# Optimization experiments

Hardware: AMD Instinct MI355X
Metric: run time of the kernel (lower is better)

## Reference

```python
import jax, jax.numpy as jnp
import numpy as np

B, T, C = 2, 2048, 2048
NH, NKVH = 16, 4
HS = C // NH  # 128
NEG_INF = -1e30


def _rope_freqs(T, hs, base=10000.0):
    inv = 1.0 / (base ** (np.arange(0, hs, 2, dtype=np.float32) / hs))  # [hs/2]
    ang = np.arange(T, dtype=np.float32)[:, None] * inv[None, :]        # [T, hs/2]
    return jnp.asarray(np.cos(ang)), jnp.asarray(np.sin(ang))


def setup_inputs() -> dict:
    key = jax.random.key(0)
    ks = jax.random.split(key, 4)
    x = jax.random.normal(ks[0], (B, T, C), dtype=jnp.float32)
    W_attn = jax.random.normal(ks[1], (C, C + 2 * NKVH * HS), dtype=jnp.float32) * 0.02
    b_attn = jnp.zeros((C + 2 * NKVH * HS,), dtype=jnp.float32)
    W_proj = jax.random.normal(ks[2], (C, C), dtype=jnp.float32) * 0.02
    b_proj = jnp.zeros((C,), dtype=jnp.float32)
    freqs_cos, freqs_sin = _rope_freqs(T, HS)
    return {"x": x, "freqs_cos": freqs_cos, "freqs_sin": freqs_sin,
            "W_attn": W_attn, "b_attn": b_attn, "W_proj": W_proj, "b_proj": b_proj}


def _apply_rope(x, cos, sin):
    # x: [B, T, H, hs]; cos/sin: [T, hs/2] -> broadcast [1, T, 1, hs/2]
    b, t, h, hs = x.shape
    x_ = x.reshape(b, t, h, hs // 2, 2)
    re, im = x_[..., 0], x_[..., 1]
    c = cos[None, :, None, :]
    s = sin[None, :, None, :]
    out_re = re * c - im * s
    out_im = re * s + im * c
    return jnp.stack([out_re, out_im], axis=-1).reshape(b, t, h, hs)


def reference(x, freqs_cos, freqs_sin, W_attn, b_attn, W_proj, b_proj):
    b, t, c = x.shape
    qkv = x @ W_attn + b_attn                                   # [B,T,C+2*nkvh*hs]
    q, k, v = jnp.split(qkv, [c, c + NKVH * HS], axis=2)
    q = q.reshape(b, t, NH, HS)
    k = k.reshape(b, t, NKVH, HS)
    v = v.reshape(b, t, NKVH, HS)
    q = _apply_rope(q, freqs_cos, freqs_sin)
    k = _apply_rope(k, freqs_cos, freqs_sin)
    # group heads: q [B, nkvh, rep, T, hs]; k,v [B, nkvh, T, hs]
    rep = NH // NKVH
    q = q.transpose(0, 2, 1, 3).reshape(b, NKVH, rep, t, HS)
    k = k.transpose(0, 2, 1, 3)
    v = v.transpose(0, 2, 1, 3)
    scale = 1.0 / jnp.sqrt(jnp.asarray(HS, dtype=x.dtype))
    scores = jnp.einsum('bgrth,bgsh->bgrts', q, k) * scale      # [B,g,rep,T,T]
    causal = jnp.tril(jnp.ones((t, t), dtype=bool))
    scores = jnp.where(causal[None, None, None], scores, NEG_INF)
    att = jax.nn.softmax(scores, axis=-1)
    y = jnp.einsum('bgrts,bgsh->bgrth', att, v)                 # [B,g,rep,T,hs]
    y = y.reshape(b, NH, t, HS).transpose(0, 2, 1, 3).reshape(b, t, c)
    return y @ W_proj + b_proj
```

## Files before the change

### kernel.cpp

```cpp
#include <hip/hip_runtime.h>
#include <hip/hip_bf16.h>
#include <stdint.h>

#define B_ 2
#define T_ 2048
#define C_ 2048
#define NH_ 16
#define NKVH_ 4
#define HS_ 128
#define QKV_ 3072
#define NTOK_ 4096

typedef __attribute__((ext_vector_type(4))) float f32x4;
typedef __attribute__((ext_vector_type(16))) float f32x16;
typedef __attribute__((ext_vector_type(8))) short s16x8;

__device__ __forceinline__ short f2bf(float f) {
    union { float f; unsigned u; } v; v.f = f;
    unsigned r = v.u + 0x7FFFu + ((v.u >> 16) & 1u);
    return (short)(r >> 16);
}

__device__ __forceinline__ void async16(const void* g, void* l) {
    __builtin_amdgcn_global_load_lds(
        (const __attribute__((address_space(1))) void*)g,
        (__attribute__((address_space(3))) void*)l, 16, 0, 0);
}

__global__ void cast_bf16_kernel(const float* __restrict__ x, short* __restrict__ out, int n8) {
    int i = blockIdx.x * 256 + threadIdx.x;
    if (i >= n8) return;
    const float4* p = (const float4*)x + (size_t)i * 2;
    float4 a = p[0], b = p[1];
    short o[8] = { f2bf(a.x), f2bf(a.y), f2bf(a.z), f2bf(a.w),
                   f2bf(b.x), f2bf(b.y), f2bf(b.z), f2bf(b.w) };
    *(int4*)(out + (size_t)i * 8) = *(const int4*)o;
}

__global__ void transcast(const float* __restrict__ W, short* __restrict__ WT, int Kd, int Nd) {
    __shared__ float tile[64][65];
    int k0 = blockIdx.x * 64, n0 = blockIdx.y * 64;
    int tid = threadIdx.x;
    int cl = tid & 63, rw = tid >> 6;
    for (int it = 0; it < 16; ++it) {
        int r = it * 4 + rw;
        tile[r][cl] = W[(size_t)(k0 + r) * Nd + n0 + cl];
    }
    __syncthreads();
    for (int it = 0; it < 16; ++it) {
        int n = it * 4 + rw;
        WT[(size_t)(n0 + n) * Kd + k0 + cl] = f2bf(tile[cl][n]);
    }
}

__global__ __launch_bounds__(256, 2) void gemm_bt(
    const short* __restrict__ A, const short* __restrict__ Bt,
    const float* __restrict__ bias, float* __restrict__ Cc,
    int M, int N, int K)
{
    __shared__ short As[128 * 64];
    __shared__ short Bs[128 * 64];
    int tid = threadIdx.x;
    int w = tid >> 6, l = tid & 63;
    int lr = l & 15, lg = l >> 4;
    int bm = blockIdx.x, bn = blockIdx.y;
    int wm = (w >> 1) * 64, wn = (w & 1) * 64;
    f32x4 acc[4][4];
#pragma unroll
    for (int i = 0; i < 4; i++)
#pragma unroll
        for (int j = 0; j < 4; j++) { acc[i][j][0]=0.f; acc[i][j][1]=0.f; acc[i][j][2]=0.f; acc[i][j][3]=0.f; }
    int arow = l >> 3, acol = (l & 7) * 8;
    for (int k0 = 0; k0 < K; k0 += 64) {
#pragma unroll
        for (int i = 0; i < 4; i++) {
            int chunk = w * 4 + i;
            int row = chunk * 8 + arow;
            async16(A  + (size_t)(bm * 128 + row) * K + k0 + acol, (char*)As + chunk * 1024);
            async16(Bt + (size_t)(bn * 128 + row) * K + k0 + acol, (char*)Bs + chunk * 1024);
        }
        __syncthreads();
#pragma unroll
        for (int ks = 0; ks < 2; ks++) {
            s16x8 af[4], bf[4];
#pragma unroll
            for (int mi = 0; mi < 4; mi++)
                af[mi] = *(const s16x8*)&As[(wm + mi * 16 + lr) * 64 + ks * 32 + lg * 8];
#pragma unroll
            for (int ni = 0; ni < 4; ni++)
                bf[ni] = *(const s16x8*)&Bs[(wn + ni * 16 + lr) * 64 + ks * 32 + lg * 8];
#pragma unroll
            for (int mi = 0; mi < 4; mi++)
#pragma unroll
                for (int ni = 0; ni < 4; ni++)
                    acc[mi][ni] = __builtin_amdgcn_mfma_f32_16x16x32_bf16(af[mi], bf[ni], acc[mi][ni], 0, 0, 0);
        }
        __syncthreads();
    }
#pragma unroll
    for (int mi = 0; mi < 4; mi++) {
        int row = bm * 128 + wm + mi * 16 + lg * 4;
#pragma unroll
        for (int ni = 0; ni < 4; ni++) {
            int col = bn * 128 + wn + ni * 16 + lr;
            float bv = bias[col];
#pragma unroll
            for (int j = 0; j < 4; j++)
                Cc[(size_t)(row + j) * N + col] = acc[mi][ni][j] + bv;
        }
    }
}

__global__ __launch_bounds__(256, 2) void gemm_qkv(
    const short* __restrict__ A, const short* __restrict__ Bt,
    const float* __restrict__ bias,
    const float* __restrict__ fcos, const float* __restrict__ fsin,
    short* __restrict__ Q, short* __restrict__ Kb, short* __restrict__ VT)
{
    __shared__ short As[128 * 64];
    __shared__ short Bs[128 * 64];
    const int K = C_;
    int tid = threadIdx.x;
    int w = tid >> 6, l = tid & 63;
    int lr = l & 15, lg = l >> 4;
    int bm = blockIdx.x, bn = blockIdx.y;
    int wm = (w >> 1) * 64, wn = (w & 1) * 64;
    f32x4 acc[4][4];
#pragma unroll
    for (int i = 0; i < 4; i++)
#pragma unroll
        for (int j = 0; j < 4; j++) { acc[i][j][0]=0.f; acc[i][j][1]=0.f; acc[i][j][2]=0.f; acc[i][j][3]=0.f; }
    int arow = l >> 3, acol = (l & 7) * 8;
    for (int k0 = 0; k0 < K; k0 += 64) {
#pragma unroll
        for (int i = 0; i < 4; i++) {
            int chunk = w * 4 + i;
            int row = chunk * 8 + arow;
            async16(A  + (size_t)(bm * 128 + row) * K + k0 + acol, (char*)As + chunk * 1024);
            async16(Bt + (size_t)(bn * 128 + row) * K + k0 + acol, (char*)Bs + chunk * 1024);
        }
        __syncthreads();
#pragma unroll
        for (int ks = 0; ks < 2; ks++) {
            s16x8 af[4], bf[4];
#pragma unroll
            for (int mi = 0; mi < 4; mi++)
                af[mi] = *(const s16x8*)&As[(wm + mi * 16 + lr) * 64 + ks * 32 + lg * 8];
#pragma unroll
            for (int ni = 0; ni < 4; ni++)
                bf[ni] = *(const s16x8*)&Bs[(wn + ni * 16 + lr) * 64 + ks * 32 + lg * 8];
#pragma unroll
            for (int mi = 0; mi < 4; mi++)
#pragma unroll
                for (int ni = 0; ni < 4; ni++)
                    acc[mi][ni] = __builtin_amdgcn_mfma_f32_16x16x32_bf16(af[mi], bf[ni], acc[mi][ni], 0, 0, 0);
        }
        __syncthreads();
    }
    int b = bm >> 4;
    int tt0 = (bm & 15) * 128 + wm;
    const float qsc = 0.08838834764831845f;
    if (bn < 20) {
        bool isQ = (bn < 16);
        short* Ob = isQ ? (Q + (size_t)(b * NH_ + bn) * T_ * HS_)
                        : (Kb + (size_t)(b * NKVH_ + (bn - 16)) * T_ * HS_);
        float sc = isQ ? qsc : 1.0f;
#pragma unroll
        for (int ni = 0; ni < 4; ni++) {
            int d = wn + ni * 16 + lr;
            int i = d >> 1;
            float ssign = (d & 1) ? 1.0f : -1.0f;
            float bv = bias[bn * 128 + d];
#pragma unroll
            for (int mi = 0; mi < 4; mi++) {
                int ttb = tt0 + mi * 16 + lg * 4;
#pragma unroll
                for (int j = 0; j < 4; j++) {
                    float v = acc[mi][ni][j] + bv;
                    float prt = __shfl_xor(v, 1);
                    int tt = ttb + j;
                    float c = fcos[tt * 64 + i], s = fsin[tt * 64 + i];
                    float outv = (v * c + ssign * prt * s) * sc;
                    Ob[(size_t)tt * HS_ + d] = f2bf(outv);
                }
            }
        }
    } else {
        int g = bn - 20;
        short* Vb = VT + (size_t)(b * NKVH_ + g) * HS_ * T_;
#pragma unroll
        for (int ni = 0; ni < 4; ni++) {
            int d = wn + ni * 16 + lr;
            float bv = bias[bn * 128 + d];
#pragma unroll
            for (int mi = 0; mi < 4; mi++) {
                int ttb = tt0 + mi * 16 + lg * 4;
                short pk4[4];
#pragma unroll
                for (int j = 0; j < 4; j++) pk4[j] = f2bf(acc[mi][ni][j] + bv);
                *(int2*)(Vb + (size_t)d * T_ + ttb) = *(const int2*)pk4;
            }
        }
    }
}

__global__ __launch_bounds__(256, 2) void attn_kernel(
    const short* __restrict__ Qg, const short* __restrict__ Kg,
    const short* __restrict__ VTg, short* __restrict__ Y)
{
    __shared__ short Ks[2][64 * 128];
    __shared__ short VTs[2][128 * 64];
    __shared__ short Ps[4][32 * 64];
    int tid = threadIdx.x, w = tid >> 6, l = tid & 63;
    int l31 = l & 31, hi = l >> 5;
    int yy = blockIdx.y;
    int qt = (yy < 8) ? yy : 23 - yy;
    int bh = blockIdx.x;
    int b = bh >> 4, h = bh & 15, g = h >> 2;
    const short* Qb = Qg + (size_t)(b * NH_ + h) * T_ * HS_;
    const short* Kb = Kg + (size_t)(b * NKVH_ + g) * T_ * HS_;
    const short* Vb = VTg + (size_t)(b * NKVH_ + g) * HS_ * T_;

    auto STAGE = [&](int st, int buf) {
#pragma unroll
        for (int i = 0; i < 4; i++) {
            int chunk = w * 4 + i;
            int poff = chunk * 1024 + l * 16;
            int qoffk = poff ^ (((poff >> 8) & 7) << 4);
            async16(Kb + (size_t)(st * 64 + (qoffk >> 8)) * HS_ + ((qoffk & 255) >> 1),
                    (char*)&Ks[buf][0] + chunk * 1024);
            int qoffv = poff ^ (((poff >> 7) & 7) << 4);
            async16(Vb + (size_t)(qoffv >> 7) * T_ + st * 64 + ((qoffv & 127) >> 1),
                    (char*)&VTs[buf][0] + chunk * 1024);
        }
    };

    int qw = qt * 128 + w * 32;
    int qglob = qw + l31;

    s16x8 qf[8];
#pragma unroll
    for (int dc = 0; dc < 8; dc++)
        qf[dc] = *(const s16x8*)(Qb + (size_t)qglob * HS_ + dc * 16 + hi * 8);

    f32x16 oacc[4];
#pragma unroll
    for (int db = 0; db < 4; db++)
#pragma unroll
        for (int i = 0; i < 16; i++) oacc[db][i] = 0.f;
    float m = -1e30f, lsum = 0.f;
    int nst = 2 * qt + 2;

    STAGE(0, 0);
    __syncthreads();
    int cur = 0;

    for (int st = 0; st < nst; ++st) {
        if (st + 1 < nst) STAGE(st + 1, cur ^ 1);
        if (st * 64 <= qw) {
            const char* KsC = (const char*)&Ks[cur][0];
            const char* VsC = (const char*)&VTs[cur][0];
            char* PsC = (char*)&Ps[w][0];

            f32x16 sacc[2];
            __builtin_amdgcn_s_setprio(1);
#pragma unroll
            for (int sb = 0; sb < 2; sb++) {
                f32x16 a0, a1;
#pragma unroll
                for (int i = 0; i < 16; i++) { a0[i] = 0.f; a1[i] = 0.f; }
#pragma unroll
                for (int dc = 0; dc < 4; dc++) {
                    int lo0 = (sb * 32 + l31) * 256 + dc * 32 + hi * 16;
                    int po0 = lo0 ^ (((lo0 >> 8) & 7) << 4);
                    s16x8 kf0 = *(const s16x8*)(KsC + po0);
                    a0 = __builtin_amdgcn_mfma_f32_32x32x16_bf16(kf0, qf[dc], a0, 0, 0, 0);
                    int lo1 = (sb * 32 + l31) * 256 + (dc + 4) * 32 + hi * 16;
                    int po1 = lo1 ^ (((lo1 >> 8) & 7) << 4);
                    s16x8 kf1 = *(const s16x8*)(KsC + po1);
                    a1 = __builtin_amdgcn_mfma_f32_32x32x16_bf16(kf1, qf[dc + 4], a1, 0, 0, 0);
                }
#pragma unroll
                for (int i = 0; i < 16; i++) a0[i] += a1[i];
                sacc[sb] = a0;
            }
            __builtin_amdgcn_s_setprio(0);
            if (st * 64 + 63 > qw) {
#pragma unroll
                for (int sb = 0; sb < 2; sb++)
#pragma unroll
                    for (int r = 0; r < 16; r++) {
                        int s = st * 64 + sb * 32 + (r & 3) + 8 * (r >> 2) + 4 * hi;
                        if (s > qglob) sacc[sb][r] = -1e30f;
                    }
            }
            float tm = -1e30f;
#pragma unroll
            for (int sb = 0; sb < 2; sb++)
#pragma unroll
                for (int r = 0; r < 16; r++) tm = fmaxf(tm, sacc[sb][r]);
            tm = fmaxf(tm, __shfl_xor(tm, 32));
            if (__any(tm > m)) {
                float mn = fmaxf(m, tm);
                float corr = __expf(m - mn);
                m = mn; lsum *= corr;
#pragma unroll
                for (int db = 0; db < 4; db++)
#pragma unroll
                    for (int r = 0; r < 16; r++) oacc[db][r] *= corr;
            }
#pragma unroll
            for (int sb = 0; sb < 2; sb++)
#pragma unroll
                for (int k = 0; k < 4; k++) {
                    float p0 = __expf(sacc[sb][4 * k]     - m);
                    float p1 = __expf(sacc[sb][4 * k + 1] - m);
                    float p2 = __expf(sacc[sb][4 * k + 2] - m);
                    float p3 = __expf(sacc[sb][4 * k + 3] - m);
                    lsum += (p0 + p1) + (p2 + p3);
                    unsigned w01 = (unsigned short)f2bf(p0) | ((unsigned)(unsigned short)f2bf(p1) << 16);
                    unsigned w23 = (unsigned short)f2bf(p2) | ((unsigned)(unsigned short)f2bf(p3) << 16);
                    uint2 pkv; pkv.x = w01; pkv.y = w23;
                    int sl = sb * 32 + 8 * k + 4 * hi;
                    int lo = l31 * 128 + sl * 2;
                    int po = lo ^ (((lo >> 7) & 7) << 4);
                    *(uint2*)(PsC + po) = pkv;
                }
            __builtin_amdgcn_s_setprio(1);
#pragma unroll
            for (int sc = 0; sc < 4; sc++) {
                unsigned ptmp[4];
                int lp = l31 * 128 + sc * 32 + hi * 16;
                int pp = lp ^ (((lp >> 7) & 7) << 4);
                *(uint2*)&ptmp[0] = *(const uint2*)(PsC + pp);
                *(uint2*)&ptmp[2] = *(const uint2*)(PsC + pp + 8);
                s16x8 pf = *(const s16x8*)ptmp;
#pragma unroll
                for (int db = 0; db < 4; db++) {
                    int lo = (db * 32 + l31) * 128 + sc * 32 + hi * 16;
                    int po = lo ^ (((lo >> 7) & 7) << 4);
                    s16x8 vf = *(const s16x8*)(VsC + po);
                    oacc[db] = __builtin_amdgcn_mfma_f32_32x32x16_bf16(vf, pf, oacc[db], 0, 0, 0);
                }
            }
            __builtin_amdgcn_s_setprio(0);
        }
        __syncthreads();
        cur ^= 1;
    }

    lsum += __shfl_xor(lsum, 32);
    float inv = 1.0f / lsum;
    short* Yrow = Y + (size_t)(b * T_ + qglob) * C_ + h * 128;
#pragma unroll
    for (int db = 0; db < 4; db++)
#pragma unroll
        for (int pr = 0; pr < 8; pr++) {
            unsigned u0 = (unsigned short)f2bf(oacc[db][2 * pr] * inv);
            unsigned u1 = (unsigned short)f2bf(oacc[db][2 * pr + 1] * inv);
            int d = db * 32 + ((2 * pr) & 3) + 8 * (pr >> 1) + 4 * hi;
            *(unsigned*)(Yrow + d) = u0 | (u1 << 16);
        }
}

extern "C" void kernel_launch(void* const* d_in, const int* in_sizes, int n_in,
                              void* d_out, int out_size, void* d_ws, size_t ws_size,
                              hipStream_t stream)
{
    const float* x      = (const float*)d_in[0];
    const float* fcos   = (const float*)d_in[1];
    const float* fsin   = (const float*)d_in[2];
    const float* W_attn = (const float*)d_in[3];
    const float* b_attn = (const float*)d_in[4];
    const float* W_proj = (const float*)d_in[5];
    const float* b_proj = (const float*)d_in[6];
    float* out = (float*)d_out;
    char* ws = (char*)d_ws;

    short* xb  = (short*)(ws + 0);
    short* y   = (short*)(ws + 16777216);
    short* WpT = (short*)(ws + 33554432);
    short* Qb  = (short*)(ws + 41943040);
    short* Kb  = (short*)(ws + 58720256);
    short* VT  = (short*)(ws + 62914560);
    short* WaT = (short*)(ws + 67108864);

    cast_bf16_kernel<<<4096, 256, 0, stream>>>(x, xb, NTOK_ * C_ / 8);
    transcast<<<dim3(32, 48), 256, 0, stream>>>(W_attn, WaT, C_, QKV_);
    gemm_qkv<<<dim3(32, 24), 256, 0, stream>>>(xb, WaT, b_attn, fcos, fsin, Qb, Kb, VT);
    transcast<<<dim3(32, 32), 256, 0, stream>>>(W_proj, WpT, C_, C_);
    attn_kernel<<<dim3(32, 16), 256, 0, stream>>>(Qb, Kb, VT, y);
    gemm_bt<<<dim3(32, 16), 256, 0, stream>>>(y, WpT, b_proj, out, NTOK_, C_, C_);
}
```

Measured before the change: 208.3 us.

## Merge prep kernels into one launch and pass P via lane shuffles

Replaces the separate activation cast and two weight transpose-cast launches with a single prep kernel that dispatches on block index, removing two launches and the gaps between them. In the attention kernel, the softmax probability tile is no longer written to and read back from a per-wave LDS buffer. Instead the packed bf16 values are kept in registers and swapped between lane halves with __shfl_xor to form the MFMA B operand. This cuts LDS traffic and shared memory use, at the cost of extra shuffle instructions and select logic.

```diff
diff --git a/kernel.cpp b/kernel.cpp
--- a/kernel.cpp
+++ b/kernel.cpp
@@ -27,20 +27,9 @@
         (__attribute__((address_space(3))) void*)l, 16, 0, 0);
 }
 
-__global__ void cast_bf16_kernel(const float* __restrict__ x, short* __restrict__ out, int n8) {
-    int i = blockIdx.x * 256 + threadIdx.x;
-    if (i >= n8) return;
-    const float4* p = (const float4*)x + (size_t)i * 2;
-    float4 a = p[0], b = p[1];
-    short o[8] = { f2bf(a.x), f2bf(a.y), f2bf(a.z), f2bf(a.w),
-                   f2bf(b.x), f2bf(b.y), f2bf(b.z), f2bf(b.w) };
-    *(int4*)(out + (size_t)i * 8) = *(const int4*)o;
-}
-
-__global__ void transcast(const float* __restrict__ W, short* __restrict__ WT, int Kd, int Nd) {
+__device__ __forceinline__ void transcast_body(const float* __restrict__ W, short* __restrict__ WT,
+                                               int Kd, int Nd, int k0, int n0, int tid) {
     __shared__ float tile[64][65];
-    int k0 = blockIdx.x * 64, n0 = blockIdx.y * 64;
-    int tid = threadIdx.x;
     int cl = tid & 63, rw = tid >> 6;
     for (int it = 0; it < 16; ++it) {
         int r = it * 4 + rw;
@@ -50,6 +39,33 @@
     for (int it = 0; it < 16; ++it) {
         int n = it * 4 + rw;
         WT[(size_t)(n0 + n) * Kd + k0 + cl] = f2bf(tile[cl][n]);
+    }
+}
+
+__global__ void prep_kernel(const float* __restrict__ x, short* __restrict__ xb,
+                            const float* __restrict__ Wa, short* __restrict__ WaT,
+                            const float* __restrict__ Wp, short* __restrict__ WpT)
+{
+    int bid = blockIdx.x, tid = threadIdx.x;
+    if (bid < 2048) {
+        const int n8 = NTOK_ * C_ / 8;
+        int i0 = bid * 512 + tid;
+#pragma unroll
+        for (int rep = 0; rep < 2; rep++) {
+            int i = i0 + rep * 256;
+            if (i >= n8) return;
+            const float4* p = (const float4*)x + (size_t)i * 2;
+            float4 a = p[0], b = p[1];
+            short o[8] = { f2bf(a.x), f2bf(a.y), f2bf(a.z), f2bf(a.w),
+                           f2bf(b.x), f2bf(b.y), f2bf(b.z), f2bf(b.w) };
+            *(int4*)(xb + (size_t)i * 8) = *(const int4*)o;
+        }
+    } else if (bid < 3584) {
+        int b2 = bid - 2048;
+        transcast_body(Wa, WaT, C_, QKV_, (b2 & 31) * 64, (b2 >> 5) * 64, tid);
+    } else {
+        int b2 = bid - 3584;
+        transcast_body(Wp, WpT, C_, C_, (b2 & 31) * 64, (b2 >> 5) * 64, tid);
     }
 }
 
@@ -210,7 +226,6 @@
 {
     __shared__ short Ks[2][64 * 128];
     __shared__ short VTs[2][128 * 64];
-    __shared__ short Ps[4][32 * 64];
     int tid = threadIdx.x, w = tid >> 6, l = tid & 63;
     int l31 = l & 31, hi = l >> 5;
     int yy = blockIdx.y;
@@ -260,7 +275,6 @@
         if (st * 64 <= qw) {
             const char* KsC = (const char*)&Ks[cur][0];
             const char* VsC = (const char*)&VTs[cur][0];
-            char* PsC = (char*)&Ps[w][0];
 
             f32x16 sacc[2];
             __builtin_amdgcn_s_setprio(1);
@@ -309,6 +323,7 @@
 #pragma unroll
                     for (int r = 0; r < 16; r++) oacc[db][r] *= corr;
             }
+            unsigned w01[2][4], w23[2][4];
 #pragma unroll
             for (int sb = 0; sb < 2; sb++)
 #pragma unroll
@@ -318,23 +333,26 @@
                     float p2 = __expf(sacc[sb][4 * k + 2] - m);
                     float p3 = __expf(sacc[sb][4 * k + 3] - m);
                     lsum += (p0 + p1) + (p2 + p3);
-                    unsigned w01 = (unsigned short)f2bf(p0) | ((unsigned)(unsigned short)f2bf(p1) << 16);
-                    unsigned w23 = (unsigned short)f2bf(p2) | ((unsigned)(unsigned short)f2bf(p3) << 16);
-                    uint2 pkv; pkv.x = w01; pkv.y = w23;
-                    int sl = sb * 32 + 8 * k + 4 * hi;
-                    int lo = l31 * 128 + sl * 2;
-                    int po = lo ^ (((lo >> 7) & 7) << 4);
-                    *(uint2*)(PsC + po) = pkv;
+                    w01[sb][k] = (unsigned)(unsigned short)f2bf(p0) | ((unsigned)(unsigned short)f2bf(p1) << 16);
+                    w23[sb][k] = (unsigned)(unsigned short)f2bf(p2) | ((unsigned)(unsigned short)f2bf(p3) << 16);
                 }
             __builtin_amdgcn_s_setprio(1);
 #pragma unroll
             for (int sc = 0; sc < 4; sc++) {
-                unsigned ptmp[4];
-                int lp = l31 * 128 + sc * 32 + hi * 16;
-                int pp = lp ^ (((lp >> 7) & 7) << 4);
-                *(uint2*)&ptmp[0] = *(const uint2*)(PsC + pp);
-                *(uint2*)&ptmp[2] = *(const uint2*)(PsC + pp + 8);
-                s16x8 pf = *(const s16x8*)ptmp;
+                const int sb = sc >> 1;
+                const int k0 = (2 * sc) & 3, k1 = k0 + 1;
+                unsigned ownA = hi ? w01[sb][k1] : w01[sb][k0];
+                unsigned ownB = hi ? w23[sb][k1] : w23[sb][k0];
+                unsigned sndA = hi ? w01[sb][k0] : w01[sb][k1];
+                unsigned sndB = hi ? w23[sb][k0] : w23[sb][k1];
+                unsigned rcvA = (unsigned)__shfl_xor((int)sndA, 32);
+                unsigned rcvB = (unsigned)__shfl_xor((int)sndB, 32);
+                unsigned uu[4];
+                uu[0] = hi ? rcvA : ownA;
+                uu[1] = hi ? rcvB : ownB;
+                uu[2] = hi ? ownA : rcvA;
+                uu[3] = hi ? ownB : rcvB;
+                s16x8 pf = *(const s16x8*)uu;
 #pragma unroll
                 for (int db = 0; db < 4; db++) {
                     int lo = (db * 32 + l31) * 128 + sc * 32 + hi * 16;
@@ -385,10 +403,8 @@
     short* VT  = (short*)(ws + 62914560);
     short* WaT = (short*)(ws + 67108864);
 
-    cast_bf16_kernel<<<4096, 256, 0, stream>>>(x, xb, NTOK_ * C_ / 8);
-    transcast<<<dim3(32, 48), 256, 0, stream>>>(W_attn, WaT, C_, QKV_);
+    prep_kernel<<<4608, 256, 0, stream>>>(x, xb, W_attn, WaT, W_proj, WpT);
     gemm_qkv<<<dim3(32, 24), 256, 0, stream>>>(xb, WaT, b_attn, fcos, fsin, Qb, Kb, VT);
-    transcast<<<dim3(32, 32), 256, 0, stream>>>(W_proj, WpT, C_, C_);
     attn_kernel<<<dim3(32, 16), 256, 0, stream>>>(Qb, Kb, VT, y);
     gemm_bt<<<dim3(32, 16), 256, 0, stream>>>(y, WpT, b_proj, out, NTOK_, C_, C_);
 }
```

After: 203.2 us (median of 2 runs). 1.03x faster.
